# Performance work log

Hardware: AMD Instinct MI355X
Metric: run time of the kernel (lower is better)

The kernel has to match this reference:

```python
import jax, jax.numpy as jnp
import numpy as np

N, M, D, K, H, W = 16, 4, 32, 256, 64, 64


def setup_inputs() -> dict:
    key = jax.random.key(0)
    kx, kc = jax.random.split(key)
    x = jax.random.normal(kx, (N, M * D, H, W), dtype=jnp.float32)
    codebook = jax.random.normal(kc, (M, K, D), dtype=jnp.float32)
    return {"x": x, "codebook": codebook}


def _distance(x, codebook):
    n, c, h, w = x.shape
    m, k, d = codebook.shape
    xr = x.reshape(n, m, d, h, w)
    x2 = jnp.sum(xr * xr, axis=2)[:, :, None]                 # (n, m, 1, h, w)
    c2 = jnp.sum(codebook * codebook, axis=-1)[None, :, :, None, None]  # (1, m, k, 1, 1)
    inter = jnp.einsum('nmdhw,mkd->nmkhw', xr, codebook)      # (n, m, k, h, w)
    dist = x2 + c2 - 2.0 * inter
    return jnp.transpose(dist, (0, 1, 3, 4, 2))               # (n, m, h, w, k)


def reference(x, codebook):
    # Faithful port of _multiCodebookQuantization.forward
    dist = _distance(x, codebook)            # squared L2 distances, (n,m,h,w,k)
    logit = jnp.log(dist)                    # torch: distance.log()
    # OneHotCategoricalStraightThrough.rsample(): hard one-hot sample
    # plus probs - stop_grad(probs) for the straight-through estimator.
    skey = jax.random.key(42)
    idx = jax.random.categorical(skey, logit, axis=-1)        # (n,m,h,w)
    hard = jax.nn.one_hot(idx, logit.shape[-1], dtype=x.dtype)
    probs = jax.nn.softmax(logit, axis=-1)
    sample = hard + probs - jax.lax.stop_gradient(probs)
    code = jnp.argmax(sample, axis=-1)
    return sample, code, logit
```

## Files before the change

kernel.cpp:

```cpp
#include <hip/hip_runtime.h>
#include <hip/hip_bf16.h>
#include <stdint.h>


#define TINY_F 1.17549435082228750797e-38f
#define LN2F   0.69314718055994530942f
#define MARGIN 4.0e-4f

constexpr int KK = 256;
constexpr int DD = 32;

typedef __attribute__((ext_vector_type(8))) short bf16x8;
typedef __attribute__((ext_vector_type(4))) float f32x4;

__device__ __forceinline__ float plog_xla(float xin) {
  #pragma clang fp contract(off)
  uint32_t ix = __float_as_uint(xin);
  int e_i = (int)(ix >> 23) - 126;
  float x = __uint_as_float((ix & 0x007FFFFFu) | 0x3F000000u);
  float e = (float)e_i;
  bool lt = x < 0.707106781186547524f;
  float tmp = lt ? x : 0.0f;
  x = x - 1.0f;
  e = e - (lt ? 1.0f : 0.0f);
  x = x + tmp;
  float z  = x * x;
  float x3 = z * x;
  float y  =  7.0376836292e-2f * x + (-1.1514610310e-1f);
  float y1 = -1.2420140846e-1f * x +   1.4249322787e-1f;
  float y2 =  2.0000714765e-1f * x + (-2.4999993993e-1f);
  y  = y  * x +   1.1676998740e-1f;
  y1 = y1 * x + (-1.6668057665e-1f);
  y2 = y2 * x +   3.3333331174e-1f;
  y  = y * x3 + y1;
  y  = y * x3 + y2;
  y  = y * x3;
  y  = y + e * (-2.12194440e-4f);
  x  = x - 0.5f * z;
  x  = x + y;
  x  = x + e * 0.693359375f;
  return x;
}

__device__ __forceinline__ float sumsq_unfused(const float* v) {
  #pragma clang fp contract(off)
  float a = 0.0f;
  #pragma unroll
  for (int d = 0; d < 32; d++) a = a + v[d] * v[d];
  return a;
}

__device__ __forceinline__ void threefry2x32(uint32_t k0, uint32_t k1,
                                             uint32_t x0, uint32_t x1,
                                             uint32_t& o0, uint32_t& o1) {
  uint32_t ks2 = k0 ^ k1 ^ 0x1BD11BDAu;
  x0 += k0; x1 += k1;
#define TF_RND(r) { x0 += x1; x1 = (x1 << (r)) | (x1 >> (32 - (r))); x1 ^= x0; }
  TF_RND(13) TF_RND(15) TF_RND(26) TF_RND(6)
  x0 += k1; x1 += ks2 + 1u;
  TF_RND(17) TF_RND(29) TF_RND(16) TF_RND(24)
  x0 += ks2; x1 += k0 + 2u;
  TF_RND(13) TF_RND(15) TF_RND(26) TF_RND(6)
  x0 += k0; x1 += k1 + 3u;
  TF_RND(17) TF_RND(29) TF_RND(16) TF_RND(24)
  x0 += k1; x1 += ks2 + 4u;
  TF_RND(13) TF_RND(15) TF_RND(26) TF_RND(6)
  x0 += ks2; x1 += k0 + 5u;
#undef TF_RND
  o0 = x0; o1 = x1;
}

__device__ __forceinline__ float gumbel_from_bits(uint32_t bits) {
  uint32_t mant = bits >> 9;
  float f = __uint_as_float(0x3F800000u | mant) - 1.0f;
  float u = mant ? f : TINY_F;
  float t = -plog_xla(u);
  return -plog_xla(t);
}

__device__ __forceinline__ float gumbel_fast(uint32_t bits) {
  uint32_t mant = bits >> 9;
  float f = __uint_as_float(0x3F800000u | mant) - 1.0f;
  float u = mant ? f : TINY_F;
  float t = -(__log2f(u) * LN2F);
  return -(__log2f(t) * LN2F);
}

__device__ __forceinline__ short bf16_rn_bits(float v) {
  __hip_bfloat16 h = __float2bfloat16(v);
  return *reinterpret_cast<short*>(&h);
}
__device__ __forceinline__ float bf16_to_f(short s) {
  __hip_bfloat16 h = *reinterpret_cast<__hip_bfloat16*>(&s);
  return __bfloat162float(h);
}

#define TRACK(P, KL, BEST, SEC, THI, I1, I2)                                   \
  if ((P) > BEST) { THI = SEC; SEC = BEST; I2 = I1; BEST = (P); I1 = (KL); }   \
  else if ((P) > SEC) { THI = SEC; SEC = (P); I2 = (KL); }                     \
  else if ((P) > THI) THI = (P);

#define EXACT_PHI_R(OUT, KI)                                                   \
  {                                                                            \
    const int _ki = (KI);                                                      \
    const float* _rp = cbm + (size_t)_ki * DD;                                 \
    float _in = 0.0f;                                                          \
    _Pragma("unroll 1")                                                        \
    for (int _j = 0; _j < 8; _j++) {                                           \
      float4 _q = *(const float4*)(_rp + (_j << 2));                           \
      _in = __builtin_fmaf(xb[(size_t)((_j<<2)+0)*4096 + hw], _q.x, _in);      \
      _in = __builtin_fmaf(xb[(size_t)((_j<<2)+1)*4096 + hw], _q.y, _in);      \
      _in = __builtin_fmaf(xb[(size_t)((_j<<2)+2)*4096 + hw], _q.z, _in);      \
      _in = __builtin_fmaf(xb[(size_t)((_j<<2)+3)*4096 + hw], _q.w, _in);      \
    }                                                                          \
    float _d = (x2e + c2m[_ki]) - 2.0f * _in;                                  \
    float _L = plog_xla(_d);                                                   \
    uint32_t _v0, _v1;                                                         \
    threefry2x32(0u, 42u, 0u, lbase | (uint32_t)_ki, _v0, _v1);                \
    OUT = gumbel_from_bits(_v0 ^ _v1) + _L;                                    \
  }

__global__ __launch_bounds__(256)
void mcq_prep(const float* __restrict__ cb, float* __restrict__ c2tab,
              short* __restrict__ cbh, short* __restrict__ cbl) {
  const int m = blockIdx.x;
  const int k = threadIdx.x;
  const float* row = cb + ((size_t)m * KK + k) * DD;
  float cr[DD];
  #pragma unroll
  for (int j = 0; j < 8; j++) {
    float4 q = ((const float4*)row)[j];
    cr[4*j+0] = q.x; cr[4*j+1] = q.y; cr[4*j+2] = q.z; cr[4*j+3] = q.w;
  }
  c2tab[m * KK + k] = sumsq_unfused(cr);
  short* hrow = cbh + ((size_t)m * KK + k) * DD;
  short* lrow = cbl + ((size_t)m * KK + k) * DD;
  #pragma unroll
  for (int d = 0; d < DD; d++) {
    float v = cr[d];
    short hb = bf16_rn_bits(v);
    float hf = bf16_to_f(hb);
    short lb = bf16_rn_bits(v - hf);
    hrow[d] = hb; lrow[d] = lb;
  }
}

__global__ __launch_bounds__(256, 8)
void mcq_mfma(const float* __restrict__ x, const float* __restrict__ cb,
              const float* __restrict__ c2tab, const short* __restrict__ cbh,
              const short* __restrict__ cbl, float* __restrict__ sample,
              float* __restrict__ code, float* __restrict__ logit) {
  __shared__ int s_wb[64];

  const int t   = threadIdx.x;
  const int l   = t & 63, wvw = t >> 6;
  const int grp = l >> 4;
  const int pbase = blockIdx.x << 6;
  const int nm  = pbase >> 12;
  const int m   = nm & 3;
  const int pxl = (wvw << 4) + (l & 15);
  const int gp  = pbase + pxl;
  const int hw  = (pbase & 4095) + pxl;

  const float* cbm = cb + (size_t)m * (KK * DD);
  const float* c2m = c2tab + m * KK;
  const short* chm = cbh + (size_t)m * (KK * DD);
  const short* clm = cbl + (size_t)m * (KK * DD);
  const float* xb  = x + (size_t)nm * 131072;

  bf16x8 bh, bl;
  float x2p = 0.0f;
  #pragma unroll
  for (int j = 0; j < 8; j++) {
    const int d = (grp << 3) + j;
    float v = xb[(size_t)d * 4096 + hw];
    short hbits = bf16_rn_bits(v);
    float hf = bf16_to_f(hbits);
    short lbits = bf16_rn_bits(v - hf);
    bh[j] = hbits; bl[j] = lbits;
    x2p = __builtin_fmaf(v, v, x2p);
  }
  x2p += __shfl_xor(x2p, 16, 64);
  x2p += __shfl_xor(x2p, 32, 64);
  const float x2f = x2p;

  float* lrowg = logit + ((size_t)gp << 8) + (grp << 2);
  const uint32_t lbase = (uint32_t)gp << 8;

  float best = -__builtin_inff(), sec = -__builtin_inff(), thi = -__builtin_inff();
  int bi1 = 0, bi2 = 0;

  #pragma unroll 1
  for (int kt = 0; kt < 16; kt++) {
    const int krow = (kt << 4) + (l & 15);
    const bf16x8 ah = *(const bf16x8*)(chm + (size_t)krow * DD + (grp << 3));
    const bf16x8 al = *(const bf16x8*)(clm + (size_t)krow * DD + (grp << 3));
    f32x4 acc = {0.0f, 0.0f, 0.0f, 0.0f};
    acc = __builtin_amdgcn_mfma_f32_16x16x32_bf16(al, bh, acc, 0, 0, 0);
    acc = __builtin_amdgcn_mfma_f32_16x16x32_bf16(ah, bl, acc, 0, 0, 0);
    acc = __builtin_amdgcn_mfma_f32_16x16x32_bf16(ah, bh, acc, 0, 0, 0);
    const float4 c2q = *(const float4*)(c2m + (kt << 4) + (grp << 2));
    const int kb = (kt << 4) + (grp << 2);

    float L0, L1, L2, L3;
#define ELEM(R, C2V, LV)                                                       \
    {                                                                          \
      float dist = (x2f + (C2V)) - 2.0f * acc[R];                              \
      LV = __log2f(dist) * LN2F;                                               \
      uint32_t v0_, v1_;                                                       \
      threefry2x32(0u, 42u, 0u, lbase | (uint32_t)(kb + (R)), v0_, v1_);       \
      float p_ = gumbel_fast(v0_ ^ v1_) + LV;                                  \
      const int kk_ = kb + (R);                                                \
      TRACK(p_, kk_, best, sec, thi, bi1, bi2)                                 \
    }
    ELEM(0, c2q.x, L0)
    ELEM(1, c2q.y, L1)
    ELEM(2, c2q.z, L2)
    ELEM(3, c2q.w, L3)
#undef ELEM
    *(float4*)(lrowg + (kt << 4)) = make_float4(L0, L1, L2, L3);
  }

#define MERGE(OFF)                                                             \
  {                                                                            \
    float ob = __shfl_xor(best, OFF, 64);                                      \
    float os = __shfl_xor(sec,  OFF, 64);                                      \
    float ot = __shfl_xor(thi,  OFF, 64);                                      \
    int  oi1 = __shfl_xor(bi1,  OFF, 64);                                      \
    int  oi2 = __shfl_xor(bi2,  OFF, 64);                                      \
    bool take = (ob > best) || (ob == best && oi1 < bi1);                      \
    float wb = take ? ob : best, ws2 = take ? os : sec, wt = take ? ot : thi;  \
    int  wi1 = take ? oi1 : bi1, wi2 = take ? oi2 : bi2;                       \
    float lb = take ? best : ob, ls = take ? sec : os;                         \
    int  li1 = take ? bi1 : oi1;                                               \
    bool s2 = (ws2 > lb) || (ws2 == lb && wi2 < li1);                          \
    best = wb; bi1 = wi1;                                                      \
    if (s2) { sec = ws2; bi2 = wi2; thi = fmaxf(wt, lb); }                     \
    else    { sec = lb;  bi2 = li1; thi = fmaxf(ws2, ls); }                    \
  }
  MERGE(16)
  MERGE(32)
#undef MERGE

  if (l < 16) {
    int w;
    if (best - sec > MARGIN) {
      w = bi1;
    } else {
      float x2e;
      {
        #pragma clang fp contract(off)
        float a = 0.0f;
        #pragma unroll 1
        for (int d = 0; d < DD; d++) {
          float v = xb[(size_t)d * 4096 + hw];
          a = a + v * v;
        }
        x2e = a;
      }
      if (best - thi > MARGIN) {
        int ka = bi1 < bi2 ? bi1 : bi2;
        int kb2 = bi1 < bi2 ? bi2 : bi1;
        float fa, fb;
        EXACT_PHI_R(fa, ka)
        EXACT_PHI_R(fb, kb2)
        w = (fb > fa) ? kb2 : ka;
      } else {
        float bb = -__builtin_inff(); int wbb = 0;
        #pragma unroll 1
        for (int k2i = 0; k2i < KK; k2i++) {
          float ph;
          EXACT_PHI_R(ph, k2i)
          if (ph > bb) { bb = ph; wbb = k2i; }
        }
        w = wbb;
      }
    }
    code[gp] = (float)w;
    s_wb[pxl] = w;
  }
  __syncthreads();

  const int k0 = l << 2;
  for (int r = wvw * 16; r < wvw * 16 + 16; r++) {
    const int wr = s_wb[r];
    float4 v;
    v.x = (wr == k0 + 0) ? 1.0f : 0.0f;
    v.y = (wr == k0 + 1) ? 1.0f : 0.0f;
    v.z = (wr == k0 + 2) ? 1.0f : 0.0f;
    v.w = (wr == k0 + 3) ? 1.0f : 0.0f;
    ((float4*)(sample + (((size_t)(pbase + r)) << 8)))[l] = v;
  }
}

extern "C" void kernel_launch(void* const* d_in, const int* in_sizes, int n_in,
                              void* d_out, int out_size, void* d_ws, size_t ws_size,
                              hipStream_t stream) {
  const float* x  = (const float*)d_in[0];
  const float* cb = (const float*)d_in[1];

  float* out_f  = (float*)d_out;
  float* sample = out_f;
  float* code   = out_f + 67108864;
  float* logit  = out_f + 67108864 + 262144;

  float* c2tab  = (float*)d_ws;
  short* cbh    = (short*)((char*)d_ws + 4096);
  short* cbl    = (short*)((char*)d_ws + 4096 + 65536);

  mcq_prep<<<4, 256, 0, stream>>>(cb, c2tab, cbh, cbl);
  mcq_mfma<<<4096, 256, 0, stream>>>(x, cb, c2tab, cbh, cbl, sample, code, logit);
}
```

Before: 220.4 us.

## Defer ambiguous-pixel exact recomputation to a separate block-parallel fixup kernel

Drops the third-best tracking and the in-kernel exact fallback paths from the main MFMA kernel. Ambiguous pixels, where the top two scores fall within the margin, are now appended to a global list via an atomic counter. A new fixup kernel then recomputes exact scores with 256 threads per pixel, one per codebook entry, and does a shared-memory argmax reduction. This removes divergent serial 256-iteration loops from the hot kernel and lightens its register pressure, at the cost of an extra launch and an atomic. Pixels beyond the list capacity would be left uncorrected.

Result: slower. 235.5 us (+6.9%).

```diff
diff --git a/kernel.cpp b/kernel.cpp
--- a/kernel.cpp
+++ b/kernel.cpp
@@ -6,6 +6,7 @@
 #define TINY_F 1.17549435082228750797e-38f
 #define LN2F   0.69314718055994530942f
 #define MARGIN 4.0e-4f
+#define LISTCAP 4096u
 
 constexpr int KK = 256;
 constexpr int DD = 32;
@@ -95,34 +96,11 @@
   return __bfloat162float(h);
 }
 
-#define TRACK(P, KL, BEST, SEC, THI, I1, I2)                                   \
-  if ((P) > BEST) { THI = SEC; SEC = BEST; I2 = I1; BEST = (P); I1 = (KL); }   \
-  else if ((P) > SEC) { THI = SEC; SEC = (P); I2 = (KL); }                     \
-  else if ((P) > THI) THI = (P);
-
-#define EXACT_PHI_R(OUT, KI)                                                   \
-  {                                                                            \
-    const int _ki = (KI);                                                      \
-    const float* _rp = cbm + (size_t)_ki * DD;                                 \
-    float _in = 0.0f;                                                          \
-    _Pragma("unroll 1")                                                        \
-    for (int _j = 0; _j < 8; _j++) {                                           \
-      float4 _q = *(const float4*)(_rp + (_j << 2));                           \
-      _in = __builtin_fmaf(xb[(size_t)((_j<<2)+0)*4096 + hw], _q.x, _in);      \
-      _in = __builtin_fmaf(xb[(size_t)((_j<<2)+1)*4096 + hw], _q.y, _in);      \
-      _in = __builtin_fmaf(xb[(size_t)((_j<<2)+2)*4096 + hw], _q.z, _in);      \
-      _in = __builtin_fmaf(xb[(size_t)((_j<<2)+3)*4096 + hw], _q.w, _in);      \
-    }                                                                          \
-    float _d = (x2e + c2m[_ki]) - 2.0f * _in;                                  \
-    float _L = plog_xla(_d);                                                   \
-    uint32_t _v0, _v1;                                                         \
-    threefry2x32(0u, 42u, 0u, lbase | (uint32_t)_ki, _v0, _v1);                \
-    OUT = gumbel_from_bits(_v0 ^ _v1) + _L;                                    \
-  }
-
 __global__ __launch_bounds__(256)
 void mcq_prep(const float* __restrict__ cb, float* __restrict__ c2tab,
-              short* __restrict__ cbh, short* __restrict__ cbl) {
+              short* __restrict__ cbh, short* __restrict__ cbl,
+              uint32_t* __restrict__ count) {
+  if (blockIdx.x == 0 && threadIdx.x == 0) *count = 0u;
   const int m = blockIdx.x;
   const int k = threadIdx.x;
   const float* row = cb + ((size_t)m * KK + k) * DD;
@@ -146,10 +124,11 @@
 }
 
 __global__ __launch_bounds__(256, 8)
-void mcq_mfma(const float* __restrict__ x, const float* __restrict__ cb,
-              const float* __restrict__ c2tab, const short* __restrict__ cbh,
-              const short* __restrict__ cbl, float* __restrict__ sample,
-              float* __restrict__ code, float* __restrict__ logit) {
+void mcq_mfma(const float* __restrict__ x, const float* __restrict__ c2tab,
+              const short* __restrict__ cbh, const short* __restrict__ cbl,
+              float* __restrict__ sample, float* __restrict__ code,
+              float* __restrict__ logit, uint32_t* __restrict__ count,
+              uint32_t* __restrict__ list) {
   __shared__ int s_wb[64];
 
   const int t   = threadIdx.x;
@@ -162,7 +141,6 @@
   const int gp  = pbase + pxl;
   const int hw  = (pbase & 4095) + pxl;
 
-  const float* cbm = cb + (size_t)m * (KK * DD);
   const float* c2m = c2tab + m * KK;
   const short* chm = cbh + (size_t)m * (KK * DD);
   const short* clm = cbl + (size_t)m * (KK * DD);
@@ -187,8 +165,8 @@
   float* lrowg = logit + ((size_t)gp << 8) + (grp << 2);
   const uint32_t lbase = (uint32_t)gp << 8;
 
-  float best = -__builtin_inff(), sec = -__builtin_inff(), thi = -__builtin_inff();
-  int bi1 = 0, bi2 = 0;
+  float best = -__builtin_inff(), sec = -__builtin_inff();
+  int bi1 = 0;
 
   #pragma unroll 1
   for (int kt = 0; kt < 16; kt++) {
@@ -210,8 +188,8 @@
       uint32_t v0_, v1_;                                                       \
       threefry2x32(0u, 42u, 0u, lbase | (uint32_t)(kb + (R)), v0_, v1_);       \
       float p_ = gumbel_fast(v0_ ^ v1_) + LV;                                  \
-      const int kk_ = kb + (R);                                                \
-      TRACK(p_, kk_, best, sec, thi, bi1, bi2)                                 \
+      if (p_ > best) { sec = best; best = p_; bi1 = kb + (R); }                \
+      else if (p_ > sec) sec = p_;                                             \
     }
     ELEM(0, c2q.x, L0)
     ELEM(1, c2q.y, L1)
@@ -221,63 +199,30 @@
     *(float4*)(lrowg + (kt << 4)) = make_float4(L0, L1, L2, L3);
   }
 
-#define MERGE(OFF)                                                             \
+#define MERGE2(OFF)                                                            \
   {                                                                            \
     float ob = __shfl_xor(best, OFF, 64);                                      \
     float os = __shfl_xor(sec,  OFF, 64);                                      \
-    float ot = __shfl_xor(thi,  OFF, 64);                                      \
     int  oi1 = __shfl_xor(bi1,  OFF, 64);                                      \
-    int  oi2 = __shfl_xor(bi2,  OFF, 64);                                      \
     bool take = (ob > best) || (ob == best && oi1 < bi1);                      \
-    float wb = take ? ob : best, ws2 = take ? os : sec, wt = take ? ot : thi;  \
-    int  wi1 = take ? oi1 : bi1, wi2 = take ? oi2 : bi2;                       \
-    float lb = take ? best : ob, ls = take ? sec : os;                         \
-    int  li1 = take ? bi1 : oi1;                                               \
-    bool s2 = (ws2 > lb) || (ws2 == lb && wi2 < li1);                          \
-    best = wb; bi1 = wi1;                                                      \
-    if (s2) { sec = ws2; bi2 = wi2; thi = fmaxf(wt, lb); }                     \
-    else    { sec = lb;  bi2 = li1; thi = fmaxf(ws2, ls); }                    \
-  }
-  MERGE(16)
-  MERGE(32)
-#undef MERGE
+    float nb  = take ? ob : best;                                              \
+    int   ni  = take ? oi1 : bi1;                                              \
+    float lsr = take ? best : ob;                            \
+    float wsr = take ? os : sec;                          \
+    best = nb; bi1 = ni;                                                       \
+    sec = fmaxf(wsr, lsr);                                                     \
+  }
+  MERGE2(16)
+  MERGE2(32)
+#undef MERGE2
 
   if (l < 16) {
-    int w;
-    if (best - sec > MARGIN) {
-      w = bi1;
-    } else {
-      float x2e;
-      {
-        #pragma clang fp contract(off)
-        float a = 0.0f;
-        #pragma unroll 1
-        for (int d = 0; d < DD; d++) {
-          float v = xb[(size_t)d * 4096 + hw];
-          a = a + v * v;
-        }
-        x2e = a;
-      }
-      if (best - thi > MARGIN) {
-        int ka = bi1 < bi2 ? bi1 : bi2;
-        int kb2 = bi1 < bi2 ? bi2 : bi1;
-        float fa, fb;
-        EXACT_PHI_R(fa, ka)
-        EXACT_PHI_R(fb, kb2)
-        w = (fb > fa) ? kb2 : ka;
-      } else {
-        float bb = -__builtin_inff(); int wbb = 0;
-        #pragma unroll 1
-        for (int k2i = 0; k2i < KK; k2i++) {
-          float ph;
-          EXACT_PHI_R(ph, k2i)
-          if (ph > bb) { bb = ph; wbb = k2i; }
-        }
-        w = wbb;
-      }
-    }
-    code[gp] = (float)w;
-    s_wb[pxl] = w;
+    code[gp] = (float)bi1;
+    s_wb[pxl] = bi1;
+    if (!(best - sec > MARGIN)) {
+      uint32_t idx = atomicAdd(count, 1u);
+      if (idx < LISTCAP) list[idx] = (uint32_t)gp;
+    }
   }
   __syncthreads();
 
@@ -293,6 +238,72 @@
   }
 }
 
+__global__ __launch_bounds__(256)
+void mcq_fix(const float* __restrict__ x, const float* __restrict__ cb,
+             const float* __restrict__ c2tab, const uint32_t* __restrict__ count,
+             const uint32_t* __restrict__ list, float* __restrict__ sample,
+             float* __restrict__ code) {
+  __shared__ unsigned long long s_scr[256];
+  const uint32_t n = min(*count, LISTCAP);
+  const int t = threadIdx.x;
+
+  for (uint32_t i = blockIdx.x; i < n; i += gridDim.x) {
+    const int gp = (int)list[i];
+    const int nm = gp >> 12;
+    const int m  = nm & 3;
+    const int hw = gp & 4095;
+    const float* cbm = cb + (size_t)m * (KK * DD);
+    const float* c2m = c2tab + m * KK;
+    const float* xb  = x + (size_t)nm * 131072;
+    const uint32_t lbase = (uint32_t)gp << 8;
+
+    float x2e;
+    {
+      #pragma clang fp contract(off)
+      float a = 0.0f;
+      #pragma unroll 1
+      for (int d = 0; d < DD; d++) {
+        float v = xb[(size_t)d * 4096 + hw];
+        a = a + v * v;
+      }
+      x2e = a;
+    }
+    float inter = 0.0f;
+    {
+      const float* rp = cbm + (size_t)t * DD;
+      #pragma unroll 1
+      for (int j = 0; j < 8; j++) {
+        float4 q = *(const float4*)(rp + (j << 2));
+        inter = __builtin_fmaf(xb[(size_t)((j<<2)+0)*4096 + hw], q.x, inter);
+        inter = __builtin_fmaf(xb[(size_t)((j<<2)+1)*4096 + hw], q.y, inter);
+        inter = __builtin_fmaf(xb[(size_t)((j<<2)+2)*4096 + hw], q.z, inter);
+        inter = __builtin_fmaf(xb[(size_t)((j<<2)+3)*4096 + hw], q.w, inter);
+      }
+    }
+    float dist = (x2e + c2m[t]) - 2.0f * inter;
+    float L = plog_xla(dist);
+    uint32_t v0, v1;
+    threefry2x32(0u, 42u, 0u, lbase | (uint32_t)t, v0, v1);
+    float phi = gumbel_from_bits(v0 ^ v1) + L;
+
+    uint32_t pb = __float_as_uint(phi);
+    pb ^= (uint32_t)(((int32_t)pb) >> 31) | 0x80000000u;
+    s_scr[t] = ((unsigned long long)pb << 32) | (unsigned long long)(255 - t);
+    __syncthreads();
+    for (int st = 128; st > 0; st >>= 1) {
+      if (t < st) {
+        unsigned long long o = s_scr[t + st];
+        if (o > s_scr[t]) s_scr[t] = o;
+      }
+      __syncthreads();
+    }
+    const int w = 255 - (int)(s_scr[0] & 0xFFu);
+    if (t == 0) code[gp] = (float)w;
+    sample[((size_t)gp << 8) + t] = (t == w) ? 1.0f : 0.0f;
+    __syncthreads();
+  }
+}
+
 extern "C" void kernel_launch(void* const* d_in, const int* in_sizes, int n_in,
                               void* d_out, int out_size, void* d_ws, size_t ws_size,
                               hipStream_t stream) {
@@ -304,10 +315,14 @@
   float* code   = out_f + 67108864;
   float* logit  = out_f + 67108864 + 262144;
 
-  float* c2tab  = (float*)d_ws;
-  short* cbh    = (short*)((char*)d_ws + 4096);
-  short* cbl    = (short*)((char*)d_ws + 4096 + 65536);
-
-  mcq_prep<<<4, 256, 0, stream>>>(cb, c2tab, cbh, cbl);
-  mcq_mfma<<<4096, 256, 0, stream>>>(x, cb, c2tab, cbh, cbl, sample, code, logit);
-}
+  float*    c2tab = (float*)d_ws;
+  short*    cbh   = (short*)((char*)d_ws + 4096);
+  short*    cbl   = (short*)((char*)d_ws + 4096 + 65536);
+  uint32_t* count = (uint32_t*)((char*)d_ws + 4096 + 131072);
+  uint32_t* list  = (uint32_t*)((char*)d_ws + 4096 + 131072 + 64);
+
+  mcq_prep<<<4, 256, 0, stream>>>(cb, c2tab, cbh, cbl, count);
+  mcq_mfma<<<4096, 256, 0, stream>>>(x, c2tab, cbh, cbl, sample, code, logit,
+                                     count, list);
+  mcq_fix<<<1024, 256, 0, stream>>>(x, cb, c2tab, count, list, sample, code);
+}
```
